# Performance work log

Measured on AMD Instinct MI355X. Metric: run time of the kernel, lower is better.

Reference implementation:

```python
import jax, jax.numpy as jnp
import numpy as np

B, C_IN, H, W = 2, 256, 48, 48
OC, G, KH, KW, PH, PW = 256, 4, 7, 7, 3, 3


def _patches(y, Hn, Wn):
    # y: (B, C, Hp, Wp) -> (B, C, KH, KW, Hn, Wn); stride=1, dilation=1
    return jnp.stack([
        jnp.stack([y[:, :, i:i + Hn, j:j + Wn] for j in range(KW)], axis=2)
        for i in range(KH)
    ], axis=2)


def setup_inputs() -> dict:
    key = jax.random.key(0)
    k1, k2, k3, k4 = jax.random.split(key, 4)
    fan_out = 3 * OC  # 1x1 conv, kaiming fan_out
    conv_w = jax.random.normal(k2, (3 * OC, C_IN), dtype=jnp.float32) * np.sqrt(2.0 / fan_out).astype(np.float32)
    return {
        "x": jax.random.normal(k1, (B, C_IN, H, W), dtype=jnp.float32),
        "conv_w": conv_w,
        "rpe_h": jax.random.normal(k3, (G, 1, KH, 1, (OC // G) // 2), dtype=jnp.float32),
        "rpe_w": jax.random.normal(k4, (G, 1, 1, KW, (OC // G) // 2), dtype=jnp.float32),
    }


def reference(x, conv_w, rpe_h, rpe_w):
    b, c, h, w = x.shape
    goc = OC // G
    c2 = goc // 2
    K = KH * KW
    center = (K - 1) // 2
    ci, cj = center // KW, center % KW

    # 1x1 conv to 3*OC channels, then zero-pad (equiv. to Conv2d(padding) + bias=False)
    y = jnp.einsum('bchw,oc->bohw', x, conv_w)
    y = jnp.pad(y, ((0, 0), (0, 0), (PH, PH), (PW, PW)))
    Hn = h + 2 * PH - (KH - 1)
    Wn = w + 2 * PW - (KW - 1)
    P = Hn * Wn

    q_full, k_full, v_full = jnp.split(y, 3, axis=1)

    # query: only the center element of each window is used
    query = q_full[:, :, ci:ci + Hn, cj:cj + Wn].reshape(b, G, goc, P)
    query = jnp.transpose(query, (0, 1, 3, 2))  # (B,G,P,goc)

    # key: full windows + relative position embeddings
    kp = _patches(k_full, Hn, Wn).reshape(b, G, goc, KH, KW, P)
    key = jnp.transpose(kp, (0, 1, 5, 3, 4, 2))  # (B,G,P,KH,KW,goc)
    key = jnp.concatenate((key[..., :c2] + rpe_h, key[..., c2:] + rpe_w), axis=1)  # (B,2G,P,KH,KW,c2)
    key = key.reshape(b, G, P, K, goc)  # row-major reshape matches torch

    vp = _patches(v_full, Hn, Wn).reshape(b, G, goc, K, P)
    value = jnp.transpose(vp, (0, 1, 4, 3, 2))  # (B,G,P,K,goc)

    att = jax.nn.softmax(jnp.einsum('bgpc,bgpkc->bgpk', query, key), axis=-1)
    out = jnp.einsum('bgpk,bgpkc->bgpc', att, value)  # (B,G,P,goc)
    out = jnp.transpose(out, (0, 1, 3, 2)).reshape(b, OC, Hn, Wn)
    return out
```

## Files before the change

kernel.cpp:

```cpp
#include <hip/hip_runtime.h>

#define BB   2
#define CIN  256
#define OC3  768
#define NG   4
#define GOC  64
#define C2   32
#define KK   49
#define PP   2304
#define HALF_P 1152

#define RS      56
#define BROWS   54
#define BSTRIDE (BROWS * RS * OC3)
#define IOFF    ((3 * RS + 3) * OC3)

#define Y2_BYTES  (BB * BROWS * RS * OC3 * 4)
#define XT_OFF    Y2_BYTES
#define WT_OFF    (XT_OFF + BB * PP * 512 * 2)

typedef __attribute__((ext_vector_type(8))) short bf16x8;
typedef __attribute__((ext_vector_type(4))) float f32x4;

struct TagH { static constexpr bool value = true;  };
struct TagW { static constexpr bool value = false; };

static __device__ __forceinline__ unsigned short f2bf_rne(float x) {
    unsigned int u = __float_as_uint(x);
    unsigned int r = u + 0x7FFFu + ((u >> 16) & 1u);
    return (unsigned short)(r >> 16);
}
static __device__ __forceinline__ float bf2f(unsigned short h) {
    return __uint_as_float(((unsigned int)h) << 16);
}

template<int CTRL>
static __device__ __forceinline__ float dpp_mov_f(float x) {
    return __int_as_float(__builtin_amdgcn_update_dpp(
        0, __float_as_int(x), CTRL, 0xF, 0xF, true));
}

#define ROW4  (RS * OC3 / 4)
#define REG1  (6 * ROW4)
#define COLS4 (OC3 / 4)
__global__ __launch_bounds__(256) void prep(
    const float* __restrict__ X, const float* __restrict__ W,
    float* __restrict__ Y2, short* __restrict__ Xt, short* __restrict__ Wt)
{
    const int bxx = blockIdx.x;
    const int tid = threadIdx.x;
    if (bxx < 1080) {
        const int b   = bxx / 540;
        const int idx = (bxx - b * 540) * 256 + tid;
        float4* Yb = (float4*)(Y2 + (size_t)b * BSTRIDE);
        const float4 z = make_float4(0.f, 0.f, 0.f, 0.f);
        if (idx < REG1) {
            int r6  = idx / ROW4;
            int rem = idx - r6 * ROW4;
            int r   = (r6 < 3) ? r6 : 48 + r6;
            Yb[r * ROW4 + rem] = z;
        } else {
            int i2  = idx - REG1;
            int r   = 3 + i2 / (8 * COLS4);
            int rem = i2 - (r - 3) * (8 * COLS4);
            int cg  = rem / COLS4;
            int c   = (cg < 3) ? cg : 48 + cg;
            int ch4 = rem - cg * COLS4;
            Yb[(r * RS + c) * COLS4 + ch4] = z;
        }
    } else if (bxx < 1848) {
        int t = (bxx - 1080) * 256 + tid;
        int o = t >> 8, c = t & 255;
        float v = W[t];
        unsigned short hi = f2bf_rne(v);
        unsigned short lo = f2bf_rne(v - bf2f(hi));
        Wt[(size_t)o * 512 + c]       = (short)hi;
        Wt[(size_t)o * 512 + 256 + c] = (short)lo;
    } else {
        __shared__ float tile[64][65];
        const int cx = bxx - 1848;
        const int p0 = (cx % 36) * 64;
        const int c0 = ((cx / 36) & 3) * 64;
        const int b  = cx / 144;
        const float* Xb = X + (size_t)b * CIN * PP;
        #pragma unroll
        for (int r = 0; r < 16; ++r) {
            int idx = r * 256 + tid;
            int c = idx >> 6, p = idx & 63;
            tile[c][p] = Xb[(size_t)(c0 + c) * PP + p0 + p];
        }
        __syncthreads();
        short* Xo = Xt + (size_t)b * PP * 512;
        #pragma unroll
        for (int r = 0; r < 16; ++r) {
            int idx = r * 256 + tid;
            int p = idx >> 6, c = idx & 63;
            float v = tile[c][p];
            unsigned short hi = f2bf_rne(v);
            unsigned short lo = f2bf_rne(v - bf2f(hi));
            size_t base = (size_t)(p0 + p) * 512 + c0 + c;
            Xo[base]       = (short)hi;
            Xo[base + 256] = (short)lo;
        }
    }
}

#define LDA 40

__global__ __launch_bounds__(256, 4) void conv_mfma(
    const short* __restrict__ Wt,
    const short* __restrict__ Xt,
    float* __restrict__ Y2)
{
    __shared__ short As[64 * LDA];
    __shared__ short Bs[64 * LDA];

    const int tid = threadIdx.x;
    const int bn  = blockIdx.x;
    const int bm  = blockIdx.y;
    const int b   = blockIdx.z;
    const int om0 = bm * 64, pn0 = bn * 64;

    const int lane = tid & 63, w = tid >> 6;
    const int oq = (w & 1) * 32, pq = (w >> 1) * 32;
    const int ln15 = lane & 15, q = lane >> 4;

    const int  lrow  = (tid & 127) >> 1;
    const int  lsoff = (tid & 1) * 16;
    const bool isA   = tid < 128;
    const short* gA = Wt + (size_t)(om0 + lrow) * 512 + lsoff;
    const short* gB = Xt + (size_t)b * PP * 512 + (size_t)(pn0 + lrow) * 512 + lsoff;
    const short* gsrc = isA ? gA : gB;
    short* ldst = (isA ? As : Bs) + lrow * LDA + lsoff;

    f32x4 acc[2][2] = {};

    for (int k0 = 0; k0 < 768; k0 += 32) {
        const int wk = (k0 < 256) ? k0 : k0 - 256;
        const int xk = (k0 < 512) ? k0 : k0 - 512;
        const int kk = isA ? wk : xk;
        uint4 v0 = *(const uint4*)(gsrc + kk);
        uint4 v1 = *(const uint4*)(gsrc + kk + 8);
        __syncthreads();
        *(uint4*)ldst       = v0;
        *(uint4*)(ldst + 8) = v1;
        __syncthreads();

        bf16x8 af[2], bf[2];
        #pragma unroll
        for (int i = 0; i < 2; ++i) {
            af[i] = *(const bf16x8*)&As[(oq + i * 16 + ln15) * LDA + q * 8];
            bf[i] = *(const bf16x8*)&Bs[(pq + i * 16 + ln15) * LDA + q * 8];
        }
        #pragma unroll
        for (int i = 0; i < 2; ++i)
            #pragma unroll
            for (int j = 0; j < 2; ++j)
                acc[i][j] = __builtin_amdgcn_mfma_f32_16x16x32_bf16(
                    af[i], bf[j], acc[i][j], 0, 0, 0);
    }

    float* Yb = Y2 + (size_t)b * BSTRIDE + IOFF;
    #pragma unroll
    for (int i = 0; i < 2; ++i) {
        #pragma unroll
        for (int j = 0; j < 2; ++j) {
            int o = om0 + oq + i * 16 + q * 4;
            int p = pn0 + pq + j * 16 + ln15;
            int h = p / 48, ww = p - h * 48;
            *(f32x4*)&Yb[(size_t)(h * RS + ww) * OC3 + o] = acc[i][j];
        }
    }
}

#define KSTR 36
__global__ __launch_bounds__(256, 4) void attn_kernel(
    const float* __restrict__ Y2,
    const float* __restrict__ rpe_h,
    const float* __restrict__ rpe_w,
    float* __restrict__ out)
{
    __shared__ float Ks[98 * KSTR];
    __shared__ float xpose[4][65];

    const int tid  = threadIdx.x;
    const int lane = tid & 63;
    const int w    = tid >> 6;
    const int bx     = blockIdx.x;
    const int wblock = (bx & 7) * 576 + (bx >> 3);
    const int wid0   = wblock * 4;
    const int pq0  = wid0 % PP;
    const int g    = (wid0 / PP) & (NG - 1);
    const int b    = wid0 / (PP * NG);
    const int ph   = pq0 / 48;
    const int pws  = pq0 - ph * 48;
    const int t    = (pq0 >= HALF_P) ? 1 : 0;
    const int qp0  = pq0 - t * HALF_P;
    const int p00  = 2 * qp0;
    const int ph0  = p00 / 48;
    const int w0   = p00 - ph0 * 48;
    const int g2   = 2 * g + t;
    const bool use_h = (g2 < NG);
    const int  kch   = use_h ? (CIN + g2 * GOC) : (CIN + (g2 - NG) * GOC + C2);
    const int  vch   = 2 * CIN + g * GOC;

    const float* Yb = Y2 + (size_t)b * BSTRIDE + IOFF;

    #pragma unroll
    for (int it = 0; it < 4; ++it) {
        int idx = it * 256 + tid;
        if (idx < 784) {
            int run = idx >> 3, f4o = idx & 7;
            int row = run / 14, col = run - row * 14;
            const float* src = Yb + (long)((ph0 + row - 3) * RS + (w0 + col - 3)) * OC3
                               + kch + f4o * 4;
            *(float4*)&Ks[run * KSTR + f4o * 4] = *(const float4*)src;
        }
    }

    const int tsub = lane >> 3;
    const int cq   = lane & 7;

    const float* qbase = Yb + (long)(ph * RS + pws + w) * OC3 + g * GOC;
    const float4 qlo = *(const float4*)(qbase + 4 * cq);
    const float4 qhi = *(const float4*)(qbase + 32 + 4 * cq);

    const float* rb = use_h ? (rpe_h + g2 * 7 * C2) : (rpe_w + (g2 - NG) * 7 * C2);
    float A0, A1, A2, A3, A4, A5, A6, H0, H1, H2, H3, H4, H5, H6;
    {
        auto rl = [&](int r, float& Ar, float& Hr) {
            float4 v = *(const float4*)(rb + r * 32 + 4 * cq);
            Ar = qlo.x * v.x + qlo.y * v.y + qlo.z * v.z + qlo.w * v.w;
            Hr = qhi.x * v.x + qhi.y * v.y + qhi.z * v.z + qhi.w * v.w;
        };
        rl(0, A0, H0); rl(1, A1, H1); rl(2, A2, H2); rl(3, A3, H3);
        rl(4, A4, H4); rl(5, A5, H5); rl(6, A6, H6);
    }
    auto selA = [&](int i) -> float {
        return i == 0 ? A0 : i == 1 ? A1 : i == 2 ? A2 :
               i == 3 ? A3 : i == 4 ? A4 : i == 5 ? A5 : A6;
    };
    auto selH = [&](int i) -> float {
        return i == 0 ? H0 : i == 1 ? H1 : i == 2 ? H2 :
               i == 3 ? H3 : i == 4 ? H4 : i == 5 ? H5 : H6;
    };

    __syncthreads();

    auto logits = [&](auto tag) -> float {
        constexpr bool UH = decltype(tag)::value;
        float lg = 0.f;
        #pragma unroll
        for (int l = 0; l < 7; ++l) {
            int kp = 8 * l + tsub;
            int m0 = 2 * kp, m1 = m0 + 1;
            int h10 = (m0 >= KK) ? 1 : 0; int k0 = m0 - KK * h10;
            int h11 = (m1 >= KK) ? 1 : 0; int k1 = m1 - KK * h11;
            int i0 = (k0 * 37) >> 8; int j0 = k0 - 7 * i0;
            int i1 = (k1 * 37) >> 8; int j1 = k1 - 7 * i1;
            int offA = (i0 * 14 + 2 * w + j0 + h10) * KSTR + 4 * cq;
            int offB = (i1 * 14 + 2 * w + j1 + h11) * KSTR + 4 * cq;
            offA = min(offA, 98 * KSTR - 4);
            offB = min(offB, 98 * KSTR - 4);
            float4 ka = *(const float4*)&Ks[offA];
            float4 kb = *(const float4*)&Ks[offB];
            float part = qlo.x * ka.x + qlo.y * ka.y + qlo.z * ka.z + qlo.w * ka.w
                       + qhi.x * kb.x + qhi.y * kb.y + qhi.z * kb.z + qhi.w * kb.w
                       + (UH ? selA(i0) : selA(j0))
                       + (UH ? selH(i1) : selH(j1));
            part += dpp_mov_f<0xB1>(part);
            part += dpp_mov_f<0x4E>(part);
            part += dpp_mov_f<0x141>(part);
            if (l == 6) part = (tsub == 0) ? part : 0.f;
            lg = (cq == l) ? part : lg;
        }
        return lg;
    };
    const float logit = use_h ? logits(TagH{}) : logits(TagW{});

    float mx = logit;
    mx = fmaxf(mx, dpp_mov_f<0xB1>(mx));
    mx = fmaxf(mx, dpp_mov_f<0x4E>(mx));
    mx = fmaxf(mx, dpp_mov_f<0x141>(mx));
    mx = fmaxf(mx, dpp_mov_f<0x128>(mx));
    mx = fmaxf(mx, __shfl_xor(mx, 16, 64));
    mx = fmaxf(mx, __shfl_xor(mx, 32, 64));
    const int Lx = 8 * cq + tsub;
    float e = (Lx < KK) ? __expf(logit - mx) : 0.f;
    float ssum = e;
    ssum += dpp_mov_f<0xB1>(ssum);
    ssum += dpp_mov_f<0x4E>(ssum);
    ssum += dpp_mov_f<0x141>(ssum);
    ssum += dpp_mov_f<0x128>(ssum);
    ssum += __shfl_xor(ssum, 16, 64);
    ssum += __shfl_xor(ssum, 32, 64);
    const float att = e / ssum;

    float acc = 0.f;
    const float* vb = Yb + (long)(ph * RS + pws + w) * OC3 + vch + lane;
    #pragma unroll
    for (int k = 0; k < KK; ++k) {
        int i = k / 7, j = k % 7;
        int doff = ((i - 3) * RS + (j - 3)) * OC3;
        int src  = 8 * (k & 7) + (k >> 3);
        float ak = __uint_as_float(
            __builtin_amdgcn_readlane(__float_as_uint(att), src));
        acc = fmaf(ak, vb[doff], acc);
    }

    xpose[w][lane] = acc;
    __syncthreads();
    const int ch = tid >> 2;
    const int w2 = tid & 3;
    out[((size_t)b * 256 + g * GOC + ch) * PP + pq0 + w2] = xpose[w2][ch];
}

extern "C" void kernel_launch(void* const* d_in, const int* in_sizes, int n_in,
                              void* d_out, int out_size, void* d_ws, size_t ws_size,
                              hipStream_t stream)
{
    const float* x  = (const float*)d_in[0];
    const float* w  = (const float*)d_in[1];
    const float* rh = (const float*)d_in[2];
    const float* rw = (const float*)d_in[3];

    float* Y2 = (float*)d_ws;
    short* Xt = (short*)((char*)d_ws + XT_OFF);
    short* Wt = (short*)((char*)d_ws + WT_OFF);

    prep<<<2136, 256, 0, stream>>>(x, w, Y2, Xt, Wt);
    conv_mfma<<<dim3(36, 12, BB), 256, 0, stream>>>(Wt, Xt, Y2);
    attn_kernel<<<(BB * NG * PP) / 4, 256, 0, stream>>>(Y2, rh, rw, (float*)d_out);
}
```

Baseline: 119.7 us.

## Drop padded Y2 buffer, bounds-check halos, restructure split-bf16 GEMM loop

Stores the 1x1 conv output unpadded (48x48), removing the zeroing of the padded border from the prep kernel and replacing padding reads with bounds checks in the attention kernel. The conv GEMM now loads hi and lo bf16 halves into separate LDS tiles and issues three MFMAs per step (hi*hi, hi*lo, lo*hi) over 256 K instead of looping over 768 concatenated K. This cuts prep work and conv loop iterations. In exchange it adds branches to the attention gather and value loops, and the LDC stride of 34 may change LDS bank-conflict behaviour.

```diff
diff --git a/kernel.cpp b/kernel.cpp
--- a/kernel.cpp
+++ b/kernel.cpp
@@ -10,12 +10,7 @@
 #define PP   2304
 #define HALF_P 1152
 
-#define RS      56
-#define BROWS   54
-#define BSTRIDE (BROWS * RS * OC3)
-#define IOFF    ((3 * RS + 3) * OC3)
-
-#define Y2_BYTES  (BB * BROWS * RS * OC3 * 4)
+#define Y2_BYTES  (BB * PP * OC3 * 4)
 #define XT_OFF    Y2_BYTES
 #define WT_OFF    (XT_OFF + BB * PP * 512 * 2)
 
@@ -40,36 +35,14 @@
         0, __float_as_int(x), CTRL, 0xF, 0xF, true));
 }
 
-#define ROW4  (RS * OC3 / 4)
-#define REG1  (6 * ROW4)
-#define COLS4 (OC3 / 4)
 __global__ __launch_bounds__(256) void prep(
     const float* __restrict__ X, const float* __restrict__ W,
-    float* __restrict__ Y2, short* __restrict__ Xt, short* __restrict__ Wt)
+    short* __restrict__ Xt, short* __restrict__ Wt)
 {
     const int bxx = blockIdx.x;
     const int tid = threadIdx.x;
-    if (bxx < 1080) {
-        const int b   = bxx / 540;
-        const int idx = (bxx - b * 540) * 256 + tid;
-        float4* Yb = (float4*)(Y2 + (size_t)b * BSTRIDE);
-        const float4 z = make_float4(0.f, 0.f, 0.f, 0.f);
-        if (idx < REG1) {
-            int r6  = idx / ROW4;
-            int rem = idx - r6 * ROW4;
-            int r   = (r6 < 3) ? r6 : 48 + r6;
-            Yb[r * ROW4 + rem] = z;
-        } else {
-            int i2  = idx - REG1;
-            int r   = 3 + i2 / (8 * COLS4);
-            int rem = i2 - (r - 3) * (8 * COLS4);
-            int cg  = rem / COLS4;
-            int c   = (cg < 3) ? cg : 48 + cg;
-            int ch4 = rem - cg * COLS4;
-            Yb[(r * RS + c) * COLS4 + ch4] = z;
-        }
-    } else if (bxx < 1848) {
-        int t = (bxx - 1080) * 256 + tid;
+    if (bxx < 768) {
+        int t = bxx * 256 + tid;
         int o = t >> 8, c = t & 255;
         float v = W[t];
         unsigned short hi = f2bf_rne(v);
@@ -78,7 +51,7 @@
         Wt[(size_t)o * 512 + 256 + c] = (short)lo;
     } else {
         __shared__ float tile[64][65];
-        const int cx = bxx - 1848;
+        const int cx = bxx - 768;
         const int p0 = (cx % 36) * 64;
         const int c0 = ((cx / 36) & 3) * 64;
         const int b  = cx / 144;
@@ -105,15 +78,17 @@
     }
 }
 
-#define LDA 40
+#define LDC 34
 
 __global__ __launch_bounds__(256, 4) void conv_mfma(
     const short* __restrict__ Wt,
     const short* __restrict__ Xt,
     float* __restrict__ Y2)
 {
-    __shared__ short As[64 * LDA];
-    __shared__ short Bs[64 * LDA];
+    __shared__ short Ah[64 * LDC];
+    __shared__ short Al[64 * LDC];
+    __shared__ short Bh[64 * LDC];
+    __shared__ short Bl[64 * LDC];
 
     const int tid = threadIdx.x;
     const int bn  = blockIdx.x;
@@ -125,50 +100,66 @@
     const int oq = (w & 1) * 32, pq = (w >> 1) * 32;
     const int ln15 = lane & 15, q = lane >> 4;
 
-    const int  lrow  = (tid & 127) >> 1;
-    const int  lsoff = (tid & 1) * 16;
-    const bool isA   = tid < 128;
-    const short* gA = Wt + (size_t)(om0 + lrow) * 512 + lsoff;
-    const short* gB = Xt + (size_t)b * PP * 512 + (size_t)(pn0 + lrow) * 512 + lsoff;
-    const short* gsrc = isA ? gA : gB;
-    short* ldst = (isA ? As : Bs) + lrow * LDA + lsoff;
+    const int arr = tid >> 6;
+    const int row = tid & 63;
+    const short* gsrc;
+    short* ldst;
+    {
+        const short* wbase = Wt + (size_t)(om0 + row) * 512;
+        const short* xbase = Xt + (size_t)b * PP * 512 + (size_t)(pn0 + row) * 512;
+        gsrc = (arr == 0) ? wbase
+             : (arr == 1) ? wbase + 256
+             : (arr == 2) ? xbase
+             :              xbase + 256;
+        short* lb = (arr == 0) ? Ah : (arr == 1) ? Al : (arr == 2) ? Bh : Bl;
+        ldst = lb + row * LDC;
+    }
 
     f32x4 acc[2][2] = {};
 
-    for (int k0 = 0; k0 < 768; k0 += 32) {
-        const int wk = (k0 < 256) ? k0 : k0 - 256;
-        const int xk = (k0 < 512) ? k0 : k0 - 512;
-        const int kk = isA ? wk : xk;
-        uint4 v0 = *(const uint4*)(gsrc + kk);
-        uint4 v1 = *(const uint4*)(gsrc + kk + 8);
+    for (int k0 = 0; k0 < 256; k0 += 32) {
+        uint4 v0 = *(const uint4*)(gsrc + k0);
+        uint4 v1 = *(const uint4*)(gsrc + k0 + 8);
+        uint4 v2 = *(const uint4*)(gsrc + k0 + 16);
+        uint4 v3 = *(const uint4*)(gsrc + k0 + 24);
         __syncthreads();
-        *(uint4*)ldst       = v0;
-        *(uint4*)(ldst + 8) = v1;
+        *(uint4*)(ldst)      = v0;
+        *(uint4*)(ldst + 8)  = v1;
+        *(uint4*)(ldst + 16) = v2;
+        *(uint4*)(ldst + 24) = v3;
         __syncthreads();
 
-        bf16x8 af[2], bf[2];
+        bf16x8 afh[2], afl[2], bfh[2], bfl[2];
         #pragma unroll
         for (int i = 0; i < 2; ++i) {
-            af[i] = *(const bf16x8*)&As[(oq + i * 16 + ln15) * LDA + q * 8];
-            bf[i] = *(const bf16x8*)&Bs[(pq + i * 16 + ln15) * LDA + q * 8];
+            int ar = (oq + i * 16 + ln15) * LDC + q * 8;
+            int br = (pq + i * 16 + ln15) * LDC + q * 8;
+            afh[i] = *(const bf16x8*)&Ah[ar];
+            afl[i] = *(const bf16x8*)&Al[ar];
+            bfh[i] = *(const bf16x8*)&Bh[br];
+            bfl[i] = *(const bf16x8*)&Bl[br];
         }
         #pragma unroll
         for (int i = 0; i < 2; ++i)
             #pragma unroll
-            for (int j = 0; j < 2; ++j)
+            for (int j = 0; j < 2; ++j) {
                 acc[i][j] = __builtin_amdgcn_mfma_f32_16x16x32_bf16(
-                    af[i], bf[j], acc[i][j], 0, 0, 0);
-    }
-
-    float* Yb = Y2 + (size_t)b * BSTRIDE + IOFF;
+                    afh[i], bfh[j], acc[i][j], 0, 0, 0);
+                acc[i][j] = __builtin_amdgcn_mfma_f32_16x16x32_bf16(
+                    afh[i], bfl[j], acc[i][j], 0, 0, 0);
+                acc[i][j] = __builtin_amdgcn_mfma_f32_16x16x32_bf16(
+                    afl[i], bfh[j], acc[i][j], 0, 0, 0);
+            }
+    }
+
+    float* Yb = Y2 + (size_t)b * PP * OC3;
     #pragma unroll
     for (int i = 0; i < 2; ++i) {
         #pragma unroll
         for (int j = 0; j < 2; ++j) {
             int o = om0 + oq + i * 16 + q * 4;
             int p = pn0 + pq + j * 16 + ln15;
-            int h = p / 48, ww = p - h * 48;
-            *(f32x4*)&Yb[(size_t)(h * RS + ww) * OC3 + o] = acc[i][j];
+            *(f32x4*)&Yb[(size_t)p * OC3 + o] = acc[i][j];
         }
     }
 }
@@ -204,7 +195,7 @@
     const int  kch   = use_h ? (CIN + g2 * GOC) : (CIN + (g2 - NG) * GOC + C2);
     const int  vch   = 2 * CIN + g * GOC;
 
-    const float* Yb = Y2 + (size_t)b * BSTRIDE + IOFF;
+    const float* Yb = Y2 + (size_t)b * PP * OC3;
 
     #pragma unroll
     for (int it = 0; it < 4; ++it) {
@@ -212,16 +203,20 @@
         if (idx < 784) {
             int run = idx >> 3, f4o = idx & 7;
             int row = run / 14, col = run - row * 14;
-            const float* src = Yb + (long)((ph0 + row - 3) * RS + (w0 + col - 3)) * OC3
-                               + kch + f4o * 4;
-            *(float4*)&Ks[run * KSTR + f4o * 4] = *(const float4*)src;
+            int gh = ph0 + row - 3;
+            int gw = w0 + col - 3;
+            float4 v = make_float4(0.f, 0.f, 0.f, 0.f);
+            if ((unsigned)gh < 48u && (unsigned)gw < 48u)
+                v = *(const float4*)(Yb + (size_t)(gh * 48 + gw) * OC3
+                                     + kch + f4o * 4);
+            *(float4*)&Ks[run * KSTR + f4o * 4] = v;
         }
     }
 
     const int tsub = lane >> 3;
     const int cq   = lane & 7;
 
-    const float* qbase = Yb + (long)(ph * RS + pws + w) * OC3 + g * GOC;
+    const float* qbase = Yb + (size_t)(ph * 48 + pws + w) * OC3 + g * GOC;
     const float4 qlo = *(const float4*)(qbase + 4 * cq);
     const float4 qhi = *(const float4*)(qbase + 32 + 4 * cq);
 
@@ -297,15 +292,18 @@
     const float att = e / ssum;
 
     float acc = 0.f;
-    const float* vb = Yb + (long)(ph * RS + pws + w) * OC3 + vch + lane;
+    const int pwv = pws + w;
+    const float* vb = Yb + (size_t)(ph * 48 + pwv) * OC3 + vch + lane;
     #pragma unroll
     for (int k = 0; k < KK; ++k) {
         int i = k / 7, j = k % 7;
-        int doff = ((i - 3) * RS + (j - 3)) * OC3;
-        int src  = 8 * (k & 7) + (k >> 3);
-        float ak = __uint_as_float(
-            __builtin_amdgcn_readlane(__float_as_uint(att), src));
-        acc = fmaf(ak, vb[doff], acc);
+        if ((unsigned)(ph + i - 3) < 48u && (unsigned)(pwv + j - 3) < 48u) {
+            int doff = ((i - 3) * 48 + (j - 3)) * OC3;
+            int src  = 8 * (k & 7) + (k >> 3);
+            float ak = __uint_as_float(
+                __builtin_amdgcn_readlane(__float_as_uint(att), src));
+            acc = fmaf(ak, vb[doff], acc);
+        }
     }
 
     xpose[w][lane] = acc;
@@ -328,7 +326,7 @@
     short* Xt = (short*)((char*)d_ws + XT_OFF);
     short* Wt = (short*)((char*)d_ws + WT_OFF);
 
-    prep<<<2136, 256, 0, stream>>>(x, w, Y2, Xt, Wt);
+    prep<<<1056, 256, 0, stream>>>(x, w, Xt, Wt);
     conv_mfma<<<dim3(36, 12, BB), 256, 0, stream>>>(Wt, Xt, Y2);
     attn_kernel<<<(BB * NG * PP) / 4, 256, 0, stream>>>(Y2, rh, rw, (float*)d_out);
 }
```

Result: slower. 140.2 us (+17.1%).
